# Kernel tuning notes

Measured on AMD Instinct MI355X. Metric: run time of the kernel, lower is better.

Reference implementation:

```python
import jax, jax.numpy as jnp
import numpy as np

EPS = 1e-5
DIM, QK, PDIM = 448, 16, 96

def _bn(y, w, b, rm, rv):
    # inference-mode BatchNorm2d over channel axis 1
    scale = (w / jnp.sqrt(rv + EPS))[None, :, None, None]
    return (y - rm[None, :, None, None]) * scale + b[None, :, None, None]

def setup_inputs() -> dict:
    key = jax.random.key(0)
    ks = jax.random.split(key, 13)
    B, H, W = 64, 32, 32
    return {
        "x": jax.random.normal(ks[0], (B, DIM, H, W), jnp.float32),
        "gn_w": jax.random.uniform(ks[1], (PDIM,), jnp.float32, 0.5, 1.5),
        "gn_b": 0.02 * jax.random.normal(ks[2], (PDIM,), jnp.float32),
        "qkv_w": jax.random.normal(ks[3], (2 * QK + PDIM, PDIM), jnp.float32) * (PDIM ** -0.5),
        "qkv_bn_w": jax.random.uniform(ks[4], (2 * QK + PDIM,), jnp.float32, 0.5, 1.5),
        "qkv_bn_b": 0.02 * jax.random.normal(ks[5], (2 * QK + PDIM,), jnp.float32),
        "qkv_bn_rm": 0.02 * jax.random.normal(ks[6], (2 * QK + PDIM,), jnp.float32),
        "qkv_bn_rv": jax.random.uniform(ks[7], (2 * QK + PDIM,), jnp.float32, 0.5, 1.5),
        "proj_w": jax.random.normal(ks[8], (DIM, DIM), jnp.float32) * (DIM ** -0.5),
        "proj_bn_w": jax.random.uniform(ks[9], (DIM,), jnp.float32, 0.5, 1.5),
        "proj_bn_b": 0.02 * jax.random.normal(ks[10], (DIM,), jnp.float32),
        "proj_bn_rm": 0.02 * jax.random.normal(ks[11], (DIM,), jnp.float32),
        "proj_bn_rv": jax.random.uniform(ks[12], (DIM,), jnp.float32, 0.5, 1.5),
    }

def reference(x, gn_w, gn_b, qkv_w, qkv_bn_w, qkv_bn_b, qkv_bn_rm, qkv_bn_rv,
              proj_w, proj_bn_w, proj_bn_b, proj_bn_rm, proj_bn_rv):
    B, C, H, W = x.shape
    scale = QK ** -0.5
    x1, x2 = x[:, :PDIM], x[:, PDIM:]
    # GroupNorm with num_groups=1: normalize over (C,H,W) per sample
    mu = jnp.mean(x1, axis=(1, 2, 3), keepdims=True)
    var = jnp.var(x1, axis=(1, 2, 3), keepdims=True)
    x1n = (x1 - mu) * jax.lax.rsqrt(var + EPS)
    x1n = x1n * gn_w[None, :, None, None] + gn_b[None, :, None, None]
    # 1x1 conv (no bias) + BN
    qkv = jnp.einsum('bchw,oc->bohw', x1n, qkv_w)
    qkv = _bn(qkv, qkv_bn_w, qkv_bn_b, qkv_bn_rm, qkv_bn_rv)
    q, k, v = qkv[:, :QK], qkv[:, QK:2 * QK], qkv[:, 2 * QK:]
    N = H * W
    q = q.reshape(B, QK, N); k = k.reshape(B, QK, N); v = v.reshape(B, PDIM, N)
    attn = jnp.einsum('bcn,bcm->bnm', q, k) * scale          # [B,N,N]
    attn = jax.nn.softmax(attn, axis=-1)
    x1o = jnp.einsum('bcm,bnm->bcn', v, attn).reshape(B, PDIM, H, W)
    y = jnp.concatenate([x1o, x2], axis=1)
    y = jax.nn.relu(y)
    y = jnp.einsum('bchw,oc->bohw', y, proj_w)
    return _bn(y, proj_bn_w, proj_bn_b, proj_bn_rm, proj_bn_rv)
```

## Files before the change

kernel.cpp:

```cpp
#include <hip/hip_runtime.h>
#include <hip/hip_bf16.h>

#define EPS 1e-5f

constexpr int BB   = 64;
constexpr int CDIM = 448;
constexpr int PD   = 96;
constexpr int QKD  = 16;
constexpr int QO   = 128;
constexpr int NPix = 1024;
constexpr int NCH  = 14;

constexpr size_t WS_MU  = 0;
constexpr size_t WS_RS  = 64;
constexpr size_t WS_QSC = 128;
constexpr size_t WS_QBI = 256;
constexpr size_t WS_PSC = 384;
constexpr size_t WS_PBI = 832;
constexpr size_t WS_WG  = 1280;
constexpr size_t WS_SWG = 13568;
constexpr size_t WS_WB  = 13696;
constexpr size_t WS_WGT = 13824;
constexpr size_t WS_WGH = 26112;
constexpr size_t WS_YB  = 32768;
constexpr size_t WS_W16 = WS_YB + (size_t)BB*NPix*CDIM/2;
constexpr size_t WS_QT  = WS_W16 + (size_t)512*CDIM/2;
constexpr size_t WS_KT  = WS_QT + (size_t)BB*NPix*32/2;
constexpr size_t WS_VB  = WS_KT + (size_t)BB*NPix*32/2;

typedef __attribute__((ext_vector_type(8))) short short8;
typedef __attribute__((ext_vector_type(8))) _Float16 half8;
typedef __attribute__((ext_vector_type(4))) float f32x4;

__device__ __forceinline__ unsigned short f2bf(float v) {
  __hip_bfloat16 h = __float2bfloat16(v);
  return *reinterpret_cast<unsigned short*>(&h);
}
__device__ __forceinline__ unsigned short f2h(float v) {
  _Float16 h = (_Float16)v;
  return *reinterpret_cast<unsigned short*>(&h);
}

typedef const __attribute__((address_space(1))) unsigned int* gp_t;
typedef __attribute__((address_space(3))) unsigned int* lp_t;
__device__ __forceinline__ void gload16(const void* g, void* l) {
  __builtin_amdgcn_global_load_lds((gp_t)g, (lp_t)l, 16, 0, 0);
}

constexpr int XT_BLOCKS = 11264;
constexpr int TAILB     = 209;
__global__ __launch_bounds__(256) void k_setup(
    const float* __restrict__ x,
    const float* __restrict__ gn_w, const float* __restrict__ gn_b,
    const float* __restrict__ qkv_w,
    const float* __restrict__ qbw, const float* __restrict__ qbb,
    const float* __restrict__ qbrm, const float* __restrict__ qbrv,
    const float* __restrict__ pw,
    const float* __restrict__ pbw, const float* __restrict__ pbb,
    const float* __restrict__ pbrm, const float* __restrict__ pbrv,
    float* __restrict__ ws, unsigned short* __restrict__ Wb,
    unsigned short* __restrict__ Ybc) {
  __shared__ float tile[32][65];
  float* red = &tile[0][0];
  int t = threadIdx.x;
  if (blockIdx.x >= TAILB) {
    int idx = blockIdx.x - TAILB;
    int nx = idx & 15, cy = (idx >> 4) % 11, b = idx / 176;
    int c0 = PD + cy * 32;
    int n0 = nx * 64;
#pragma unroll
    for (int i = 0; i < 2; ++i) {
      int k = t + i * 256;
      int c = k >> 4, q = k & 15;
      float4 v = reinterpret_cast<const float4*>(
                     x + ((size_t)b * CDIM + c0 + c) * NPix + n0)[q];
      *reinterpret_cast<float4*>(&tile[c][q * 4]) = v;
    }
    __syncthreads();
    int n = t >> 2, ch = t & 3;
    short8 o;
#pragma unroll
    for (int j = 0; j < 8; ++j)
      o[j] = (short)f2bf(fmaxf(tile[ch * 8 + j][n], 0.f));
    *reinterpret_cast<short8*>(
        &Ybc[(((size_t)b * NCH + 3 + cy) * NPix + n0 + n) * 32 + ch * 8]) = o;
    return;
  }
  int bid = blockIdx.x;
  if (bid < 64) {
    int b = bid;
    const float4* x4 = reinterpret_cast<const float4*>(x + (size_t)b * CDIM * NPix);
    float s = 0.f, ss = 0.f;
#pragma unroll 8
    for (int ii = 0; ii < PD * NPix / 4 / 256; ++ii) {
      float4 v = x4[t + ii * 256];
      s  += v.x + v.y + v.z + v.w;
      ss += v.x * v.x + v.y * v.y + v.z * v.z + v.w * v.w;
    }
#pragma unroll
    for (int o = 32; o > 0; o >>= 1) { s += __shfl_down(s, o); ss += __shfl_down(ss, o); }
    int wid = t >> 6;
    if ((t & 63) == 0) { red[wid] = s; red[4 + wid] = ss; }
    __syncthreads();
    if (t == 0) {
      float S  = red[0] + red[1] + red[2] + red[3];
      float SS = red[4] + red[5] + red[6] + red[7];
      const float inv_n = 1.f / (PD * NPix);
      float mu  = S * inv_n;
      float var = SS * inv_n - mu * mu;
      ws[WS_MU + b] = mu;
      ws[WS_RS + b] = rsqrtf(var + EPS);
    }
  } else if (bid < 96) {
    int o = (bid - 64) * 4 + (t >> 6);
    int lane = t & 63;
    unsigned short* Wgh = reinterpret_cast<unsigned short*>(ws + WS_WGH);
    float sw = 0.f, bb = 0.f;
    for (int c = lane; c < PD; c += 64) {
      float w  = qkv_w[o * PD + c];
      float wg = w * gn_w[c];
      Wgh[(size_t)o * PD + c] = f2h(wg);
      sw += wg;
      bb += w * gn_b[c];
    }
#pragma unroll
    for (int off = 32; off > 0; off >>= 1) {
      sw += __shfl_down(sw, off);
      bb += __shfl_down(bb, off);
    }
    if (lane == 0) {
      ws[WS_SWG + o] = sw;
      ws[WS_WB + o]  = bb;
      float sc = qbw[o] * rsqrtf(qbrv[o] + EPS);
      ws[WS_QSC + o] = sc;
      ws[WS_QBI + o] = qbb[o] - qbrm[o] * sc;
    }
  } else if (bid == 96) {
    for (int o = t; o < CDIM; o += 256) {
      float sc = pbw[o] * rsqrtf(pbrv[o] + EPS);
      ws[WS_PSC + o] = sc;
      ws[WS_PBI + o] = pbb[o] - pbrm[o] * sc;
    }
  } else {
    int idx = (bid - 97) * 256 + t;
    int row = idx / 56, sl = (idx % 56) * 8;
    short8 o = {};
    if (row < CDIM) {
      const float* src = pw + (size_t)row * CDIM + sl;
#pragma unroll
      for (int j = 0; j < 8; ++j) o[j] = (short)f2bf(src[j]);
    }
    *reinterpret_cast<short8*>(&Wb[(size_t)row * CDIM + sl]) = o;
  }
}

__global__ __launch_bounds__(256) void k_qkv2(const float* __restrict__ x,
                                              float* __restrict__ ws,
                                              unsigned short* __restrict__ qt,
                                              unsigned short* __restrict__ kt,
                                              unsigned short* __restrict__ vb) {
  __shared__ __align__(16) char smem[PD * 132 * 4];
  float*          xt = reinterpret_cast<float*>(smem);
  unsigned short* ld = reinterpret_cast<unsigned short*>(smem);

  int lin = blockIdx.x + 8 * blockIdx.y;
  int swz = (lin & 7) * 64 + (lin >> 3);
  int n0  = (swz & 7) * 128;
  int b   = swz >> 3;
  int t   = threadIdx.x;
  int lane = t & 63, w = t >> 6;
  int lo = lane & 15, hi = lane >> 4;

  const float4* xb4 = reinterpret_cast<const float4*>(x + (size_t)b * CDIM * NPix);
#pragma unroll
  for (int i = 0; i < 12; ++i) {
    int idx = t + i * 256;
    int row = idx >> 5, c4 = idx & 31;
    float4 v = xb4[row * (NPix / 4) + (n0 >> 2) + c4];
    *reinterpret_cast<float4*>(&xt[row * 132 + c4 * 4]) = v;
  }
  __syncthreads();

  const unsigned short* Wgh = reinterpret_cast<const unsigned short*>(ws + WS_WGH);
  f32x4 acc[8][2] = {{{}}};
#pragma unroll
  for (int kk = 0; kk < 3; ++kk) {
    half8 bfr[2];
#pragma unroll
    for (int nf = 0; nf < 2; ++nf) {
      int nr = w * 32 + nf * 16 + lo;
      half8 h;
#pragma unroll
      for (int j = 0; j < 8; ++j)
        h[j] = (_Float16)xt[(kk * 32 + hi * 8 + j) * 132 + nr];
      bfr[nf] = h;
    }
#pragma unroll
    for (int of = 0; of < 8; ++of) {
      half8 a = *reinterpret_cast<const half8*>(
          &Wgh[(size_t)(of * 16 + lo) * PD + kk * 32 + hi * 8]);
      acc[of][0] = __builtin_amdgcn_mfma_f32_16x16x32_f16(a, bfr[0], acc[of][0], 0, 0, 0);
      acc[of][1] = __builtin_amdgcn_mfma_f32_16x16x32_f16(a, bfr[1], acc[of][1], 0, 0, 0);
    }
  }
  float mu = ws[WS_MU + b], rs = ws[WS_RS + b];
  __syncthreads();
#pragma unroll
  for (int of = 0; of < 8; ++of) {
#pragma unroll
    for (int r = 0; r < 4; ++r) {
      int o = of * 16 + hi * 4 + r;
      float bias = ws[WS_WB + o] - rs * mu * ws[WS_SWG + o];
      float qs = ws[WS_QSC + o], qb = ws[WS_QBI + o];
      float postm = (o < QKD) ? 0.25f : 1.f;
#pragma unroll
      for (int nf = 0; nf < 2; ++nf) {
        int nl = w * 32 + nf * 16 + lo;
        float v = (qs * (rs * acc[of][nf][r] + bias) + qb) * postm;
        ld[o * 136 + nl] = f2h(v);
      }
    }
  }
  __syncthreads();
#pragma unroll
  for (int i = 0; i < 6; ++i) {
    int idx = t + i * 256;
    int row = idx >> 4, c8 = idx & 15;
    short8 v = *reinterpret_cast<const short8*>(&ld[(32 + row) * 136 + c8 * 8]);
    *reinterpret_cast<short8*>(&vb[((size_t)b * PD + row) * NPix + n0 + c8 * 8]) = v;
  }
#pragma unroll
  for (int i = 0; i < 4; ++i) {
    int idx = t + i * 256;
    int arr = idx >> 9;
    int rem = idx & 511;
    int n = rem >> 2, q4 = rem & 3;
    short8 o = {};
    if (q4 < 2) {
#pragma unroll
      for (int j = 0; j < 8; ++j)
        o[j] = (short)ld[(arr * 16 + q4 * 8 + j) * 136 + n];
    }
    unsigned short* dst = arr ? kt : qt;
    *reinterpret_cast<short8*>(&dst[((size_t)b * NPix + n0 + n) * 32 + q4 * 8]) = o;
  }
}

__global__ __launch_bounds__(512) void k_attn2(
    const unsigned short* __restrict__ qt,
    const unsigned short* __restrict__ kt,
    const unsigned short* __restrict__ vb,
    unsigned short* __restrict__ Ybc) {
  __shared__ __align__(16) unsigned short kt_s[128 * 40];
  __shared__ __align__(16) unsigned short vt_s[96 * 136];
  __shared__ __align__(16) unsigned short P_s[8 * 16 * 136];

  int lin = blockIdx.x + 8 * blockIdx.y;
  int swz = (lin & 7) * 64 + (lin >> 3);
  int n0  = (swz & 7) * 128;
  int b   = swz >> 3;
  int t  = threadIdx.x;
  int lane = t & 63, w = t >> 6;
  int lo = lane & 15, hi = lane >> 4;

  half8 q8 = *reinterpret_cast<const half8*>(
      &qt[((size_t)b * NPix + n0 + w * 16 + lo) * 32 + hi * 8]);

  const unsigned short* ktb = kt + (size_t)b * NPix * 32;
  const unsigned short* vbb = vb + (size_t)b * PD * NPix;

  f32x4 o[6] = {};
  float M = -1e30f, L = 0.f;
  f32x4 zero = {};

  for (int mt = 0; mt < 8; ++mt) {
    int m0 = mt * 128;
    int krow = t >> 2, kc4 = t & 3;
    float4 rk = *reinterpret_cast<const float4*>(&ktb[(size_t)(m0 + krow) * 32 + kc4 * 8]);
    float4 rv[3];
#pragma unroll
    for (int i = 0; i < 3; ++i) {
      int ci = t + 512 * i;
      int row = ci >> 4, c4 = ci & 15;
      rv[i] = *reinterpret_cast<const float4*>(&vbb[(size_t)row * NPix + m0 + c4 * 8]);
    }
    __syncthreads();
    *reinterpret_cast<float4*>(&kt_s[krow * 40 + kc4 * 8]) = rk;
#pragma unroll
    for (int i = 0; i < 3; ++i) {
      int ci = t + 512 * i;
      int row = ci >> 4, c4 = ci & 15;
      *reinterpret_cast<float4*>(&vt_s[row * 136 + c4 * 8]) = rv[i];
    }
    __syncthreads();

    f32x4 s[8];
    __builtin_amdgcn_s_setprio(1);
#pragma unroll
    for (int ss = 0; ss < 8; ++ss) {
      half8 a = *reinterpret_cast<const half8*>(&kt_s[(ss * 16 + lo) * 40 + hi * 8]);
      s[ss] = __builtin_amdgcn_mfma_f32_16x16x32_f16(a, q8, zero, 0, 0, 0);
    }
    __builtin_amdgcn_s_setprio(0);

    float tmax = s[0][0];
#pragma unroll
    for (int ss = 0; ss < 8; ++ss)
#pragma unroll
      for (int r = 0; r < 4; ++r) tmax = fmaxf(tmax, s[ss][r]);
    tmax = fmaxf(tmax, __shfl_xor(tmax, 16));
    tmax = fmaxf(tmax, __shfl_xor(tmax, 32));
    float newM = fmaxf(M, tmax);
    float fac = __expf(M - newM);
    M = newM;
    float psum = 0.f;
    unsigned pbase = (w * 16 + lo) * 136;
#pragma unroll
    for (int ss = 0; ss < 8; ++ss) {
      float p0 = __expf(s[ss][0] - M);
      float p1 = __expf(s[ss][1] - M);
      float p2 = __expf(s[ss][2] - M);
      float p3 = __expf(s[ss][3] - M);
      psum += (p0 + p1) + (p2 + p3);
      unsigned u01 = (unsigned)f2h(p0) | ((unsigned)f2h(p1) << 16);
      unsigned u23 = (unsigned)f2h(p2) | ((unsigned)f2h(p3) << 16);
      *reinterpret_cast<unsigned*>(&P_s[pbase + 16 * ss + 4 * hi])     = u01;
      *reinterpret_cast<unsigned*>(&P_s[pbase + 16 * ss + 4 * hi + 2]) = u23;
    }
    psum += __shfl_xor(psum, 16);
    psum += __shfl_xor(psum, 32);
    L = L * fac + psum;
#pragma unroll
    for (int cf = 0; cf < 6; ++cf)
#pragma unroll
      for (int r = 0; r < 4; ++r) o[cf][r] *= fac;
    asm volatile("s_waitcnt lgkmcnt(0)" ::: "memory");

    __builtin_amdgcn_s_setprio(1);
#pragma unroll
    for (int ks = 0; ks < 4; ++ks) {
      half8 pb = *reinterpret_cast<const half8*>(&P_s[pbase + ks * 32 + hi * 8]);
#pragma unroll
      for (int cf = 0; cf < 6; ++cf) {
        half8 va = *reinterpret_cast<const half8*>(&vt_s[(cf * 16 + lo) * 136 + ks * 32 + hi * 8]);
        o[cf] = __builtin_amdgcn_mfma_f32_16x16x32_f16(va, pb, o[cf], 0, 0, 0);
      }
    }
    __builtin_amdgcn_s_setprio(0);
  }

  float inv = 1.f / L;
  unsigned pbase = (w * 16 + lo) * 136;
#pragma unroll
  for (int cf = 0; cf < 6; ++cf) {
    float v0 = fmaxf(o[cf][0] * inv, 0.f);
    float v1 = fmaxf(o[cf][1] * inv, 0.f);
    float v2 = fmaxf(o[cf][2] * inv, 0.f);
    float v3 = fmaxf(o[cf][3] * inv, 0.f);
    unsigned u01 = (unsigned)f2bf(v0) | ((unsigned)f2bf(v1) << 16);
    unsigned u23 = (unsigned)f2bf(v2) | ((unsigned)f2bf(v3) << 16);
    *reinterpret_cast<unsigned*>(&P_s[pbase + cf * 16 + 4 * hi])     = u01;
    *reinterpret_cast<unsigned*>(&P_s[pbase + cf * 16 + 4 * hi + 2]) = u23;
  }
  asm volatile("s_waitcnt lgkmcnt(0)" ::: "memory");
#pragma unroll
  for (int j = 0; j < 3; ++j) {
    int k = lane + 64 * j;
    int n = k / 12, c8 = k % 12;
    short8 vv = *reinterpret_cast<const short8*>(&P_s[(w * 16 + n) * 136 + c8 * 8]);
    *reinterpret_cast<short8*>(
        &Ybc[(((size_t)b * NCH + (c8 >> 2)) * NPix + n0 + w * 16 + n) * 32
             + (c8 & 3) * 8]) = vv;
  }
}

__global__ __launch_bounds__(256) void k_projmm(
    const unsigned short* __restrict__ Wb,
    const unsigned short* __restrict__ Ybc,
    const float* __restrict__ ws,
    float* __restrict__ out) {
  __shared__ __align__(16) unsigned short At[3][128 * 32];
  int lin = blockIdx.x + 8 * (blockIdx.y + 4 * blockIdx.z);
  int swz = (lin & 7) * 256 + (lin >> 3);
  int m0  = (swz & 3) * 128;
  int n0  = ((swz >> 2) & 7) * 128;
  int b   = swz >> 5;
  int t  = threadIdx.x;
  int lane = t & 63, wid = t >> 6;
  int wm = wid >> 1, wn = wid & 1;
  int lo = lane & 15, hi = lane >> 4;

  const unsigned short* Arow = Wb + (size_t)m0 * CDIM;
  const unsigned short* Brow = Ybc + ((size_t)b * NCH * NPix + n0) * 32;

  int chunk0 = wid * 128 + lane;
  int row0 = chunk0 >> 2, sl0 = (chunk0 & 3) ^ ((row0 >> 1) & 3);
  int chunk1 = chunk0 + 64;
  int row1 = chunk1 >> 2, sl1 = (chunk1 & 3) ^ ((row1 >> 1) & 3);

#define STAGE_A(bufi, s_)                                                      \
  do {                                                                         \
    gload16(Arow + (size_t)row0 * CDIM + (s_) * 32 + sl0 * 8,                  \
            &At[bufi][(wid * 128) * 8]);                                       \
    gload16(Arow + (size_t)row1 * CDIM + (s_) * 32 + sl1 * 8,                  \
            &At[bufi][(wid * 128 + 64) * 8]);                                  \
  } while (0)

#define LOADB(dst, s_)                                                         \
  do {                                                                         \
    _Pragma("unroll")                                                          \
    for (int f = 0; f < 4; ++f)                                                \
      dst[f] = *reinterpret_cast<const short8*>(                               \
          &Brow[(size_t)(s_) * NPix * 32 + (wn * 64 + f * 16 + lo) * 32 +      \
                hi * 8]);                                                      \
  } while (0)

  f32x4 acc[4][4] = {{{}}};
  short8 bcur[4], bnxt[4];

  STAGE_A(0, 0);
  STAGE_A(1, 1);
  LOADB(bcur, 0);
  asm volatile("s_waitcnt vmcnt(6)" ::: "memory");
  __builtin_amdgcn_sched_barrier(0);
  __builtin_amdgcn_s_barrier();

#pragma unroll
  for (int s = 0; s < 14; ++s) {
    if (s + 2 <= 13) STAGE_A((s + 2) % 3, s + 2);
    if (s + 1 <= 13) LOADB(bnxt, s + 1);
    short8 af[4];
#pragma unroll
    for (int f = 0; f < 4; ++f) {
      int ar = wm * 64 + f * 16 + lo;
      int as = hi ^ ((ar >> 1) & 3);
      af[f] = *reinterpret_cast<const short8*>(&At[s % 3][ar * 32 + as * 8]);
    }
#pragma unroll
    for (int i = 0; i < 4; ++i)
#pragma unroll
      for (int j = 0; j < 4; ++j)
        acc[i][j] = __builtin_amdgcn_mfma_f32_16x16x32_bf16(af[i], bcur[j], acc[i][j], 0, 0, 0);
#pragma unroll
    for (int f = 0; f < 4; ++f) bcur[f] = bnxt[f];
    if (s < 13) {
      if (s <= 11) asm volatile("s_waitcnt vmcnt(6) lgkmcnt(0)" ::: "memory");
      else         asm volatile("s_waitcnt vmcnt(4) lgkmcnt(0)" ::: "memory");
      __builtin_amdgcn_sched_barrier(0);
      __builtin_amdgcn_s_barrier();
    }
  }
#undef STAGE_A
#undef LOADB

  int col = lane & 15, rq = lane >> 4;
#pragma unroll
  for (int i = 0; i < 4; ++i) {
    int ob = m0 + wm * 64 + i * 16 + rq * 4;
#pragma unroll
    for (int r = 0; r < 4; ++r) {
      int o = ob + r;
      if (o < CDIM) {
        float ps = ws[WS_PSC + o], pb = ws[WS_PBI + o];
        size_t base = ((size_t)b * CDIM + o) * NPix + n0 + wn * 64 + col;
#pragma unroll
        for (int j = 0; j < 4; ++j)
          out[base + j * 16] = ps * acc[i][j][r] + pb;
      }
    }
  }
}

extern "C" void kernel_launch(void* const* d_in, const int* in_sizes, int n_in,
                              void* d_out, int out_size, void* d_ws, size_t ws_size,
                              hipStream_t stream) {
  const float* x      = (const float*)d_in[0];
  const float* gn_w   = (const float*)d_in[1];
  const float* gn_b   = (const float*)d_in[2];
  const float* qkv_w  = (const float*)d_in[3];
  const float* qbw    = (const float*)d_in[4];
  const float* qbb    = (const float*)d_in[5];
  const float* qbrm   = (const float*)d_in[6];
  const float* qbrv   = (const float*)d_in[7];
  const float* pw     = (const float*)d_in[8];
  const float* pbw    = (const float*)d_in[9];
  const float* pbb    = (const float*)d_in[10];
  const float* pbrm   = (const float*)d_in[11];
  const float* pbrv   = (const float*)d_in[12];
  float* out = (float*)d_out;
  float* ws  = (float*)d_ws;
  unsigned short* Ybc = (unsigned short*)(ws + WS_YB);
  unsigned short* Wb  = (unsigned short*)(ws + WS_W16);
  unsigned short* qt  = (unsigned short*)(ws + WS_QT);
  unsigned short* kt  = (unsigned short*)(ws + WS_KT);
  unsigned short* vb  = (unsigned short*)(ws + WS_VB);

  k_setup<<<TAILB + XT_BLOCKS, 256, 0, stream>>>(
      x, gn_w, gn_b, qkv_w, qbw, qbb, qbrm, qbrv,
      pw, pbw, pbb, pbrm, pbrv, ws, Wb, Ybc);
  k_qkv2<<<dim3(8, BB), 256, 0, stream>>>(x, ws, qt, kt, vb);
  k_attn2<<<dim3(8, BB), 512, 0, stream>>>(qt, kt, vb, Ybc);
  k_projmm<<<dim3(8, 4, BB), 256, 0, stream>>>(Wb, Ybc, ws, out);
}
```

Before: 138.1 us.

## Split x2 ReLU transpose into qkv and attention kernels, halve query tiles, drop LDS staging

The x2 channel ReLU/bf16 transpose blocks move out of the setup kernel. Half of them (batches 0-31) now run as extra blocks in the qkv kernel and the other half (batches 32-63) as extra blocks in the attention kernel, so this bandwidth-bound work can overlap with compute-heavy blocks. The qkv and attention kernels now use 64-pixel query tiles with 256 threads, giving 1024 main blocks instead of 512. The attention kernel also stops staging K and V tiles through LDS with barriers and reads MFMA operands straight from global memory, trading redundant global/L2 traffic for fewer syncs and less shared memory.

```diff
diff --git a/kernel.cpp b/kernel.cpp
--- a/kernel.cpp
+++ b/kernel.cpp
@@ -47,8 +47,7 @@
   __builtin_amdgcn_global_load_lds((gp_t)g, (lp_t)l, 16, 0, 0);
 }
 
-constexpr int XT_BLOCKS = 11264;
-constexpr int TAILB     = 209;
+constexpr int TAILB = 209;
 __global__ __launch_bounds__(256) void k_setup(
     const float* __restrict__ x,
     const float* __restrict__ gn_w, const float* __restrict__ gn_b,
@@ -58,34 +57,9 @@
     const float* __restrict__ pw,
     const float* __restrict__ pbw, const float* __restrict__ pbb,
     const float* __restrict__ pbrm, const float* __restrict__ pbrv,
-    float* __restrict__ ws, unsigned short* __restrict__ Wb,
-    unsigned short* __restrict__ Ybc) {
-  __shared__ float tile[32][65];
-  float* red = &tile[0][0];
+    float* __restrict__ ws, unsigned short* __restrict__ Wb) {
+  __shared__ float red[8];
   int t = threadIdx.x;
-  if (blockIdx.x >= TAILB) {
-    int idx = blockIdx.x - TAILB;
-    int nx = idx & 15, cy = (idx >> 4) % 11, b = idx / 176;
-    int c0 = PD + cy * 32;
-    int n0 = nx * 64;
-#pragma unroll
-    for (int i = 0; i < 2; ++i) {
-      int k = t + i * 256;
-      int c = k >> 4, q = k & 15;
-      float4 v = reinterpret_cast<const float4*>(
-                     x + ((size_t)b * CDIM + c0 + c) * NPix + n0)[q];
-      *reinterpret_cast<float4*>(&tile[c][q * 4]) = v;
-    }
-    __syncthreads();
-    int n = t >> 2, ch = t & 3;
-    short8 o;
-#pragma unroll
-    for (int j = 0; j < 8; ++j)
-      o[j] = (short)f2bf(fmaxf(tile[ch * 8 + j][n], 0.f));
-    *reinterpret_cast<short8*>(
-        &Ybc[(((size_t)b * NCH + 3 + cy) * NPix + n0 + n) * 32 + ch * 8]) = o;
-    return;
-  }
   int bid = blockIdx.x;
   if (bid < 64) {
     int b = bid;
@@ -158,49 +132,69 @@
                                               float* __restrict__ ws,
                                               unsigned short* __restrict__ qt,
                                               unsigned short* __restrict__ kt,
-                                              unsigned short* __restrict__ vb) {
-  __shared__ __align__(16) char smem[PD * 132 * 4];
+                                              unsigned short* __restrict__ vb,
+                                              unsigned short* __restrict__ Ybc) {
+  __shared__ __align__(16) char smem[PD * 68 * 4];
   float*          xt = reinterpret_cast<float*>(smem);
   unsigned short* ld = reinterpret_cast<unsigned short*>(smem);
-
-  int lin = blockIdx.x + 8 * blockIdx.y;
-  int swz = (lin & 7) * 64 + (lin >> 3);
-  int n0  = (swz & 7) * 128;
-  int b   = swz >> 3;
-  int t   = threadIdx.x;
+  int t = threadIdx.x;
+
+  if (blockIdx.x >= 1024) {
+    int idx = (int)blockIdx.x - 1024;
+    int nx = idx & 15, cy = (idx >> 4) % 11, bb = idx / 176;
+    int c0 = PD + cy * 32;
+    int n0x = nx * 64;
+    float* txt = reinterpret_cast<float*>(smem);
+#pragma unroll
+    for (int i = 0; i < 2; ++i) {
+      int k = t + i * 256;
+      int c = k >> 4, q = k & 15;
+      float4 v = reinterpret_cast<const float4*>(
+                     x + ((size_t)bb * CDIM + c0 + c) * NPix + n0x)[q];
+      *reinterpret_cast<float4*>(&txt[c * 65 + q * 4]) = v;
+    }
+    __syncthreads();
+    int n = t >> 2, ch = t & 3;
+    short8 o;
+#pragma unroll
+    for (int j = 0; j < 8; ++j)
+      o[j] = (short)f2bf(fmaxf(txt[(ch * 8 + j) * 65 + n], 0.f));
+    *reinterpret_cast<short8*>(
+        &Ybc[(((size_t)bb * NCH + 3 + cy) * NPix + n0x + n) * 32 + ch * 8]) = o;
+    return;
+  }
+
+  int lin = blockIdx.x;
+  int swz = (lin & 7) * 128 + (lin >> 3);
+  int n0  = (swz & 15) * 64;
+  int b   = swz >> 4;
   int lane = t & 63, w = t >> 6;
   int lo = lane & 15, hi = lane >> 4;
 
   const float4* xb4 = reinterpret_cast<const float4*>(x + (size_t)b * CDIM * NPix);
 #pragma unroll
-  for (int i = 0; i < 12; ++i) {
+  for (int i = 0; i < 6; ++i) {
     int idx = t + i * 256;
-    int row = idx >> 5, c4 = idx & 31;
+    int row = idx >> 4, c4 = idx & 15;
     float4 v = xb4[row * (NPix / 4) + (n0 >> 2) + c4];
-    *reinterpret_cast<float4*>(&xt[row * 132 + c4 * 4]) = v;
+    *reinterpret_cast<float4*>(&xt[row * 68 + c4 * 4]) = v;
   }
   __syncthreads();
 
   const unsigned short* Wgh = reinterpret_cast<const unsigned short*>(ws + WS_WGH);
-  f32x4 acc[8][2] = {{{}}};
+  f32x4 acc[8] = {{}};
+  int nr = w * 16 + lo;
 #pragma unroll
   for (int kk = 0; kk < 3; ++kk) {
-    half8 bfr[2];
-#pragma unroll
-    for (int nf = 0; nf < 2; ++nf) {
-      int nr = w * 32 + nf * 16 + lo;
-      half8 h;
-#pragma unroll
-      for (int j = 0; j < 8; ++j)
-        h[j] = (_Float16)xt[(kk * 32 + hi * 8 + j) * 132 + nr];
-      bfr[nf] = h;
-    }
+    half8 h;
+#pragma unroll
+    for (int j = 0; j < 8; ++j)
+      h[j] = (_Float16)xt[(kk * 32 + hi * 8 + j) * 68 + nr];
 #pragma unroll
     for (int of = 0; of < 8; ++of) {
       half8 a = *reinterpret_cast<const half8*>(
           &Wgh[(size_t)(of * 16 + lo) * PD + kk * 32 + hi * 8]);
-      acc[of][0] = __builtin_amdgcn_mfma_f32_16x16x32_f16(a, bfr[0], acc[of][0], 0, 0, 0);
-      acc[of][1] = __builtin_amdgcn_mfma_f32_16x16x32_f16(a, bfr[1], acc[of][1], 0, 0, 0);
+      acc[of] = __builtin_amdgcn_mfma_f32_16x16x32_f16(a, h, acc[of], 0, 0, 0);
     }
   }
   float mu = ws[WS_MU + b], rs = ws[WS_RS + b];
@@ -213,53 +207,73 @@
       float bias = ws[WS_WB + o] - rs * mu * ws[WS_SWG + o];
       float qs = ws[WS_QSC + o], qb = ws[WS_QBI + o];
       float postm = (o < QKD) ? 0.25f : 1.f;
-#pragma unroll
-      for (int nf = 0; nf < 2; ++nf) {
-        int nl = w * 32 + nf * 16 + lo;
-        float v = (qs * (rs * acc[of][nf][r] + bias) + qb) * postm;
-        ld[o * 136 + nl] = f2h(v);
-      }
+      float v = (qs * (rs * acc[of][r] + bias) + qb) * postm;
+      ld[o * 72 + nr] = f2h(v);
     }
   }
   __syncthreads();
 #pragma unroll
-  for (int i = 0; i < 6; ++i) {
+  for (int i = 0; i < 3; ++i) {
     int idx = t + i * 256;
-    int row = idx >> 4, c8 = idx & 15;
-    short8 v = *reinterpret_cast<const short8*>(&ld[(32 + row) * 136 + c8 * 8]);
+    int row = idx >> 3, c8 = idx & 7;
+    short8 v = *reinterpret_cast<const short8*>(&ld[(32 + row) * 72 + c8 * 8]);
     *reinterpret_cast<short8*>(&vb[((size_t)b * PD + row) * NPix + n0 + c8 * 8]) = v;
   }
 #pragma unroll
-  for (int i = 0; i < 4; ++i) {
+  for (int i = 0; i < 2; ++i) {
     int idx = t + i * 256;
-    int arr = idx >> 9;
-    int rem = idx & 511;
+    int arr = idx >> 8;
+    int rem = idx & 255;
     int n = rem >> 2, q4 = rem & 3;
     short8 o = {};
     if (q4 < 2) {
 #pragma unroll
       for (int j = 0; j < 8; ++j)
-        o[j] = (short)ld[(arr * 16 + q4 * 8 + j) * 136 + n];
+        o[j] = (short)ld[(arr * 16 + q4 * 8 + j) * 72 + n];
     }
     unsigned short* dst = arr ? kt : qt;
     *reinterpret_cast<short8*>(&dst[((size_t)b * NPix + n0 + n) * 32 + q4 * 8]) = o;
   }
 }
 
-__global__ __launch_bounds__(512) void k_attn2(
+__global__ __launch_bounds__(256) void k_attn2(
+    const float* __restrict__ x,
     const unsigned short* __restrict__ qt,
     const unsigned short* __restrict__ kt,
     const unsigned short* __restrict__ vb,
     unsigned short* __restrict__ Ybc) {
-  __shared__ __align__(16) unsigned short kt_s[128 * 40];
-  __shared__ __align__(16) unsigned short vt_s[96 * 136];
-  __shared__ __align__(16) unsigned short P_s[8 * 16 * 136];
-
-  int lin = blockIdx.x + 8 * blockIdx.y;
-  int swz = (lin & 7) * 64 + (lin >> 3);
-  int n0  = (swz & 7) * 128;
-  int b   = swz >> 3;
-  int t  = threadIdx.x;
+  __shared__ __align__(16) unsigned short P_s[64 * 136];
+  int t = threadIdx.x;
+
+  if (blockIdx.x >= 1024) {
+    int idx = (int)blockIdx.x - 1024;
+    int nx = idx & 15, cy = (idx >> 4) % 11, bb = 32 + idx / 176;
+    int c0 = PD + cy * 32;
+    int n0x = nx * 64;
+    float* txt = reinterpret_cast<float*>(P_s);
+#pragma unroll
+    for (int i = 0; i < 2; ++i) {
+      int k = t + i * 256;
+      int c = k >> 4, q = k & 15;
+      float4 v = reinterpret_cast<const float4*>(
+                     x + ((size_t)bb * CDIM + c0 + c) * NPix + n0x)[q];
+      *reinterpret_cast<float4*>(&txt[c * 65 + q * 4]) = v;
+    }
+    __syncthreads();
+    int n = t >> 2, ch = t & 3;
+    short8 o;
+#pragma unroll
+    for (int j = 0; j < 8; ++j)
+      o[j] = (short)f2bf(fmaxf(txt[(ch * 8 + j) * 65 + n], 0.f));
+    *reinterpret_cast<short8*>(
+        &Ybc[(((size_t)bb * NCH + 3 + cy) * NPix + n0x + n) * 32 + ch * 8]) = o;
+    return;
+  }
+
+  int lin = blockIdx.x;
+  int swz = (lin & 7) * 128 + (lin >> 3);
+  int n0  = (swz & 15) * 64;
+  int b   = swz >> 4;
   int lane = t & 63, w = t >> 6;
   int lo = lane & 15, hi = lane >> 4;
 
@@ -272,33 +286,16 @@
   f32x4 o[6] = {};
   float M = -1e30f, L = 0.f;
   f32x4 zero = {};
+  unsigned pbase = (w * 16 + lo) * 136;
 
   for (int mt = 0; mt < 8; ++mt) {
     int m0 = mt * 128;
-    int krow = t >> 2, kc4 = t & 3;
-    float4 rk = *reinterpret_cast<const float4*>(&ktb[(size_t)(m0 + krow) * 32 + kc4 * 8]);
-    float4 rv[3];
-#pragma unroll
-    for (int i = 0; i < 3; ++i) {
-      int ci = t + 512 * i;
-      int row = ci >> 4, c4 = ci & 15;
-      rv[i] = *reinterpret_cast<const float4*>(&vbb[(size_t)row * NPix + m0 + c4 * 8]);
-    }
-    __syncthreads();
-    *reinterpret_cast<float4*>(&kt_s[krow * 40 + kc4 * 8]) = rk;
-#pragma unroll
-    for (int i = 0; i < 3; ++i) {
-      int ci = t + 512 * i;
-      int row = ci >> 4, c4 = ci & 15;
-      *reinterpret_cast<float4*>(&vt_s[row * 136 + c4 * 8]) = rv[i];
-    }
-    __syncthreads();
-
     f32x4 s[8];
     __builtin_amdgcn_s_setprio(1);
 #pragma unroll
     for (int ss = 0; ss < 8; ++ss) {
-      half8 a = *reinterpret_cast<const half8*>(&kt_s[(ss * 16 + lo) * 40 + hi * 8]);
+      half8 a = *reinterpret_cast<const half8*>(
+          &ktb[(size_t)(m0 + ss * 16 + lo) * 32 + hi * 8]);
       s[ss] = __builtin_amdgcn_mfma_f32_16x16x32_f16(a, q8, zero, 0, 0, 0);
     }
     __builtin_amdgcn_s_setprio(0);
@@ -314,7 +311,6 @@
     float fac = __expf(M - newM);
     M = newM;
     float psum = 0.f;
-    unsigned pbase = (w * 16 + lo) * 136;
 #pragma unroll
     for (int ss = 0; ss < 8; ++ss) {
       float p0 = __expf(s[ss][0] - M);
@@ -342,7 +338,8 @@
       half8 pb = *reinterpret_cast<const half8*>(&P_s[pbase + ks * 32 + hi * 8]);
 #pragma unroll
       for (int cf = 0; cf < 6; ++cf) {
-        half8 va = *reinterpret_cast<const half8*>(&vt_s[(cf * 16 + lo) * 136 + ks * 32 + hi * 8]);
+        half8 va = *reinterpret_cast<const half8*>(
+            &vbb[(size_t)(cf * 16 + lo) * NPix + m0 + ks * 32 + hi * 8]);
         o[cf] = __builtin_amdgcn_mfma_f32_16x16x32_f16(va, pb, o[cf], 0, 0, 0);
       }
     }
@@ -350,7 +347,6 @@
   }
 
   float inv = 1.f / L;
-  unsigned pbase = (w * 16 + lo) * 136;
 #pragma unroll
   for (int cf = 0; cf < 6; ++cf) {
     float v0 = fmaxf(o[cf][0] * inv, 0.f);
@@ -495,10 +491,10 @@
   unsigned short* kt  = (unsigned short*)(ws + WS_KT);
   unsigned short* vb  = (unsigned short*)(ws + WS_VB);
 
-  k_setup<<<TAILB + XT_BLOCKS, 256, 0, stream>>>(
+  k_setup<<<TAILB, 256, 0, stream>>>(
       x, gn_w, gn_b, qkv_w, qbw, qbb, qbrm, qbrv,
-      pw, pbw, pbb, pbrm, pbrv, ws, Wb, Ybc);
-  k_qkv2<<<dim3(8, BB), 256, 0, stream>>>(x, ws, qt, kt, vb);
-  k_attn2<<<dim3(8, BB), 512, 0, stream>>>(qt, kt, vb, Ybc);
+      pw, pbw, pbb, pbrm, pbrv, ws, Wb);
+  k_qkv2<<<1024 + 5632, 256, 0, stream>>>(x, ws, qt, kt, vb, Ybc);
+  k_attn2<<<1024 + 5632, 256, 0, stream>>>(x, qt, kt, vb, Ybc);
   k_projmm<<<dim3(8, 4, BB), 256, 0, stream>>>(Wb, Ybc, ws, out);
 }
```

After: 206.1 us. 49.2% more time.
